# Optimization experiments

Hardware: AMD Instinct MI355X
Metric: run time of the kernel (lower is better)

Reference implementation:

```python
import jax, jax.numpy as jnp
import numpy as np
from jax import lax

B, H_IN, W_IN = 64, 480, 80
HID = 256                      # feature_dimension / 2
T = H_IN // 12                 # hidden_shape[0] = 40
I_GRU = (W_IN // 4) * 32       # hidden_shape[1] = 640


def setup_inputs() -> dict:
    key = jax.random.key(0)
    ks = jax.random.split(key, 20)
    rn = lambda k, s, sc: jax.random.normal(k, s, jnp.float32) * sc
    gs = 1.0 / np.sqrt(HID)    # torch GRU default init scale
    return {
        "input_image": jax.random.normal(ks[0], (B, 1, H_IN, W_IN), jnp.float32),
        "hidden": jnp.zeros((2, B, HID), jnp.float32),
        # conv weights: module uses randn*0.2 via init_conv_weights
        "conv0_w": rn(ks[1], (8, 1, 3, 3), 0.2),   "conv0_b": rn(ks[2], (8,), 0.05),
        "conv1_w": rn(ks[3], (16, 8, 3, 3), 0.2),  "conv1_b": rn(ks[4], (16,), 0.05),
        "conv2_w": rn(ks[5], (16, 16, 3, 3), 0.2), "conv2_b": rn(ks[6], (16,), 0.05),
        "conv3_w": rn(ks[7], (32, 16, 3, 3), 0.2), "conv3_b": rn(ks[8], (32,), 0.05),
        # GRU (1 layer, bidirectional). gate order: r, z, n (torch convention)
        "w_ih_f": rn(ks[9], (3 * HID, I_GRU), gs), "w_hh_f": rn(ks[10], (3 * HID, HID), gs),
        "b_ih_f": rn(ks[11], (3 * HID,), gs),      "b_hh_f": rn(ks[12], (3 * HID,), gs),
        "w_ih_b": rn(ks[13], (3 * HID, I_GRU), gs), "w_hh_b": rn(ks[14], (3 * HID, HID), gs),
        "b_ih_b": rn(ks[15], (3 * HID,), gs),       "b_hh_b": rn(ks[16], (3 * HID,), gs),
    }


def _conv(x, w, b):
    y = lax.conv_general_dilated(x, w, (1, 1), ((1, 1), (1, 1)),
                                 dimension_numbers=("NCHW", "OIHW", "NCHW"))
    return y + b[None, :, None, None]


def _maxpool(x, kh, kw):
    return lax.reduce_window(x, -jnp.inf, lax.max,
                             (1, 1, kh, kw), (1, 1, kh, kw), "VALID")


def _gru_dir(x_tbi, h0, w_ih, w_hh, b_ih, b_hh):
    # x_tbi: [T, B, I]; precompute input-side gates for all steps
    gx = jnp.einsum("tbi,gi->tbg", x_tbi, w_ih) + b_ih  # [T, B, 3H]

    def step(h, gx_t):
        gh = h @ w_hh.T + b_hh                            # [B, 3H]
        xr, xz, xn = jnp.split(gx_t, 3, axis=-1)
        hr, hz, hn = jnp.split(gh, 3, axis=-1)
        r = jax.nn.sigmoid(xr + hr)
        z = jax.nn.sigmoid(xz + hz)
        n = jnp.tanh(xn + r * hn)
        h_new = (1.0 - z) * n + z * h
        return h_new, h_new

    hT, ys = lax.scan(step, h0, gx)
    return ys, hT  # ys: [T, B, H]


def reference(input_image, hidden,
              conv0_w, conv0_b, conv1_w, conv1_b,
              conv2_w, conv2_b, conv3_w, conv3_b,
              w_ih_f, w_hh_f, b_ih_f, b_hh_f,
              w_ih_b, w_hh_b, b_ih_b, b_hh_b):
    y0 = jax.nn.relu(_conv(input_image, conv0_w, conv0_b))
    y1 = jax.nn.relu(_conv(y0, conv1_w, conv1_b))
    y2 = _maxpool(y1, 3, 2)
    y3 = jax.nn.relu(_conv(y2, conv2_w, conv2_b))
    y4 = jax.nn.relu(_conv(y3, conv3_w, conv3_b))
    y5 = _maxpool(y4, 4, 2)                     # [B, 32, T, W']
    b = y5.shape[0]
    # Python-loop reshape y_out[:, :, i] = y5[:, i%32, :, i//32]
    # is exactly a NCHW->NHWC permute followed by flattening (W', C):
    gru_in = jnp.transpose(y5, (0, 2, 3, 1)).reshape(b, T, I_GRU)
    x = jnp.transpose(gru_in, (1, 0, 2))        # [T, B, I]
    ys_f, hT_f = _gru_dir(x, hidden[0], w_ih_f, w_hh_f, b_ih_f, b_hh_f)
    ys_b, hT_b = _gru_dir(x[::-1], hidden[1], w_ih_b, w_hh_b, b_ih_b, b_hh_b)
    ys_b = ys_b[::-1]
    output = jnp.transpose(jnp.concatenate([ys_f, ys_b], axis=-1), (1, 0, 2))  # [B, T, 2H]
    hidden_out = jnp.stack([hT_f, hT_b], axis=0)                               # [2, B, H]
    return output, hidden_out
```

## Files before the change

kernel.cpp:

```cpp
#include <hip/hip_runtime.h>
#include <math.h>

static constexpr int B_   = 64;
static constexpr int H0_  = 480, W0_ = 80;
static constexpr int C0_  = 8, C1_ = 16, C2_ = 16, C3_ = 32;
static constexpr int H1_  = 160, W1_ = 40;
static constexpr int T_   = 40,  WP_ = 20;
static constexpr int IG_  = 640;
static constexpr int HID_ = 256;
static constexpr int G3_  = 768;
static constexpr int OUT_MAIN_ = B_ * T_ * 2 * HID_;
static constexpr int WSZ_ = G3_ * IG_;

typedef __attribute__((ext_vector_type(8))) short bf16x8;
typedef __attribute__((ext_vector_type(4))) short s16x4;
typedef __attribute__((ext_vector_type(4))) float f32x4;

__device__ inline short f2bf(float f) {
  unsigned u = __builtin_bit_cast(unsigned, f);
  u = (u + 0x7FFFu + ((u >> 16) & 1u)) >> 16;
  return (short)u;
}
__device__ inline float bf2f(short s) {
  return __builtin_bit_cast(float, ((unsigned)(unsigned short)s) << 16);
}
__device__ inline float sigm_(float x) { return 1.f / (1.f + __expf(-x)); }
__device__ inline float tanh_(float x) { return 1.f - 2.f / (1.f + __expf(2.f * x)); }

__device__ inline void split8(const float* p, bf16x8* hi, bf16x8* lo) {
  float4 u = *(const float4*)p, v = *(const float4*)(p + 4);
  float f[8] = {u.x, u.y, u.z, u.w, v.x, v.y, v.z, v.w};
  bf16x8 h, l;
#pragma unroll
  for (int i = 0; i < 8; ++i) {
    short hs = f2bf(f[i]);
    h[i] = hs;
    l[i] = f2bf(f[i] - bf2f(hs));
  }
  *hi = h; *lo = l;
}

__global__ __launch_bounds__(512, 4) void conv01_mfma(
    const float* __restrict__ img, const float* __restrict__ w0,
    const float* __restrict__ b0, const float* __restrict__ w1,
    const float* __restrict__ b1, float* __restrict__ y2) {
  __shared__ __align__(16) float im[16 * 84];
  __shared__ __align__(16) short y0h[14 * 82 * 8];
  __shared__ __align__(16) short y0l[14 * 82 * 8];
  int b = blockIdx.x / 40, tb = blockIdx.x % 40;
  int tid = threadIdx.x;
  int wave = tid >> 6, lane = tid & 63, q = lane >> 4, m15 = lane & 15;
  const float* imgb = img + (size_t)b * (H0_ * W0_);

  for (int i = tid; i < 16 * 84; i += 512) {
    int r = i / 84, col = i % 84;
    int gr = tb * 12 - 2 + r, gc = col - 2;
    float v = 0.f;
    if (gr >= 0 && gr < H0_ && gc >= 0 && gc < W0_) v = imgb[gr * W0_ + gc];
    im[i] = v;
  }
  bf16x8 w1hf[3], w1lf[3];
#pragma unroll
  for (int kt = 0; kt < 3; ++kt) {
    int p = kt * 4 + q;
    bf16x8 h, l;
#pragma unroll
    for (int e = 0; e < 8; ++e) {
      float w = (p < 9) ? w1[m15 * 72 + e * 9 + p] : 0.f;
      short hs = f2bf(w);
      h[e] = hs;
      l[e] = f2bf(w - bf2f(hs));
    }
    w1hf[kt] = h; w1lf[kt] = l;
  }
  float b1c = b1[m15];
  __syncthreads();

  {
    int ci = tid & 7;
    float wv0[9];
#pragma unroll
    for (int k = 0; k < 9; ++k) wv0[k] = w0[ci * 9 + k];
    float b0c = b0[ci];
#pragma unroll 1
    for (int i = tid; i < 14 * 82 * 8; i += 512) {
      int rest = i >> 3;
      int lc = rest % 82, r = rest / 82;
      int grow = tb * 12 - 1 + r, gc = lc - 1;
      float v = 0.f;
      if (grow >= 0 && grow < H0_ && gc >= 0 && gc < W0_) {
        float s = b0c;
#pragma unroll
        for (int kh = 0; kh < 3; ++kh)
#pragma unroll
          for (int kw = 0; kw < 3; ++kw)
            s += im[(r + kh) * 84 + lc + kw] * wv0[kh * 3 + kw];
        v = fmaxf(s, 0.f);
      }
      short hs = f2bf(v);
      y0h[i] = hs;
      y0l[i] = f2bf(v - bf2f(hs));
    }
  }
  __syncthreads();

#pragma unroll 1
  for (int j = wave; j < 20; j += 8) {
    int pr = j / 5, ct = j % 5;
    f32x4 pmax = {0.f, 0.f, 0.f, 0.f};
#pragma unroll
    for (int rr2 = 0; rr2 < 3; ++rr2) {
      int o = pr * 3 + rr2;
      f32x4 acc = {0.f, 0.f, 0.f, 0.f};
#pragma unroll
      for (int kt = 0; kt < 3; ++kt) {
        int p = kt * 4 + q;
        int pp = (p < 9) ? p : 8;
        int kh = pp / 3, kw = pp % 3;
        int ar = ((o + kh) * 82 + ct * 16 + m15 + kw) * 8;
        bf16x8 ah = *(const bf16x8*)&y0h[ar];
        bf16x8 al = *(const bf16x8*)&y0l[ar];
        acc = __builtin_amdgcn_mfma_f32_16x16x32_bf16(al, w1hf[kt], acc, 0, 0, 0);
        acc = __builtin_amdgcn_mfma_f32_16x16x32_bf16(ah, w1lf[kt], acc, 0, 0, 0);
        acc = __builtin_amdgcn_mfma_f32_16x16x32_bf16(ah, w1hf[kt], acc, 0, 0, 0);
      }
#pragma unroll
      for (int r = 0; r < 4; ++r)
        pmax[r] = fmaxf(pmax[r], fmaxf(acc[r] + b1c, 0.f));
    }
    int R = tb * 4 + pr;
    size_t base = (((size_t)b * 160 + R) * 40 + ct * 8 + q * 2) * 16 + m15;
    y2[base] = fmaxf(pmax[0], pmax[1]);
    y2[base + 16] = fmaxf(pmax[2], pmax[3]);
  }
}

__global__ __launch_bounds__(512, 2) void conv23_mfma(
    const float* __restrict__ y2, const float* __restrict__ w2,
    const float* __restrict__ b2, const float* __restrict__ w3,
    const float* __restrict__ b3, short* __restrict__ xh,
    short* __restrict__ xl) {
  __shared__ __align__(16) short y2h[20 * 42 * 16], y2l[20 * 42 * 16];
  __shared__ __align__(16) short y3h[18 * 42 * 16], y3l[18 * 42 * 16];
  int b = blockIdx.x / 10, tb = blockIdx.x % 10;
  int tid = threadIdx.x;
  int wave = tid >> 6, lane = tid & 63, q = lane >> 4, m15 = lane & 15;
  int ci0 = (q & 1) * 8;

  for (int i = tid; i < 20 * 42 * 4; i += 512) {
    int ci4 = i & 3;
    int rest = i >> 2;
    int lc = rest % 42, r = rest / 42;
    int gr = tb * 16 - 2 + r, gc = lc - 1;
    float4 v = {0.f, 0.f, 0.f, 0.f};
    if (gr >= 0 && gr < 160 && gc >= 0 && gc < 40)
      v = *(const float4*)&y2[(((size_t)b * 160 + gr) * 40 + gc) * 16 + ci4 * 4];
    float f[4] = {v.x, v.y, v.z, v.w};
    s16x4 hv, lv;
#pragma unroll
    for (int e = 0; e < 4; ++e) {
      short hs = f2bf(f[e]);
      hv[e] = hs;
      lv[e] = f2bf(f[e] - bf2f(hs));
    }
    int idx = (r * 42 + lc) * 16 + ci4 * 4;
    *(s16x4*)&y2h[idx] = hv;
    *(s16x4*)&y2l[idx] = lv;
  }
  for (int i = tid; i < 18 * 2 * 16; i += 512) {
    int rr = i / 32, sl = i % 32;
    int col = (sl >> 4) * 41, ch = sl & 15;
    y3h[(rr * 42 + col) * 16 + ch] = 0;
    y3l[(rr * 42 + col) * 16 + ch] = 0;
  }
  bf16x8 w2hf[5], w2lf[5];
#pragma unroll
  for (int kt = 0; kt < 5; ++kt) {
    int p = 2 * kt + (q >> 1);
    bf16x8 h, l;
#pragma unroll
    for (int e = 0; e < 8; ++e) {
      float w = (p < 9) ? w2[(m15 * 16 + ci0 + e) * 9 + p] : 0.f;
      short hs = f2bf(w);
      h[e] = hs;
      l[e] = f2bf(w - bf2f(hs));
    }
    w2hf[kt] = h; w2lf[kt] = l;
  }
  float b2c = b2[m15];
  __syncthreads();

#pragma unroll 1
  for (int i = wave; i < 54; i += 8) {
    int rr = i / 3, ct = i % 3;
    f32x4 acc = {0.f, 0.f, 0.f, 0.f};
#pragma unroll
    for (int kt = 0; kt < 5; ++kt) {
      int p = 2 * kt + (q >> 1);
      int pp = (p < 9) ? p : 8;
      int kh = pp / 3, kw = pp % 3;
      int lc = min(ct * 16 + m15 + kw, 41);
      int ar = ((rr + kh) * 42 + lc) * 16 + ci0;
      bf16x8 ah = *(const bf16x8*)&y2h[ar];
      bf16x8 al = *(const bf16x8*)&y2l[ar];
      acc = __builtin_amdgcn_mfma_f32_16x16x32_bf16(al, w2hf[kt], acc, 0, 0, 0);
      acc = __builtin_amdgcn_mfma_f32_16x16x32_bf16(ah, w2lf[kt], acc, 0, 0, 0);
      acc = __builtin_amdgcn_mfma_f32_16x16x32_bf16(ah, w2hf[kt], acc, 0, 0, 0);
    }
    int grow = tb * 16 - 1 + rr;
    bool rowok = (grow >= 0 && grow < 160);
#pragma unroll
    for (int r = 0; r < 4; ++r) {
      int col = ct * 16 + q * 4 + r;
      if (col < 40) {
        float v = rowok ? fmaxf(acc[r] + b2c, 0.f) : 0.f;
        short hs = f2bf(v);
        int di = (rr * 42 + 1 + col) * 16 + m15;
        y3h[di] = hs;
        y3l[di] = f2bf(v - bf2f(hs));
      }
    }
  }
  __syncthreads();

  int nt = wave & 1, pl = wave >> 1;
  bf16x8 w3hf[5], w3lf[5];
#pragma unroll
  for (int kt = 0; kt < 5; ++kt) {
    int p = 2 * kt + (q >> 1);
    bf16x8 h, l;
#pragma unroll
    for (int e = 0; e < 8; ++e) {
      float w = (p < 9) ? w3[((nt * 16 + m15) * 16 + ci0 + e) * 9 + p] : 0.f;
      short hs = f2bf(w);
      h[e] = hs;
      l[e] = f2bf(w - bf2f(hs));
    }
    w3hf[kt] = h; w3lf[kt] = l;
  }
  float b3c = b3[nt * 16 + m15];

#pragma unroll 1
  for (int ct = 0; ct < 3; ++ct) {
    f32x4 pmax = {0.f, 0.f, 0.f, 0.f};
#pragma unroll
    for (int rr2 = 0; rr2 < 4; ++rr2) {
      int o = pl * 4 + rr2;
      f32x4 acc = {0.f, 0.f, 0.f, 0.f};
#pragma unroll
      for (int kt = 0; kt < 5; ++kt) {
        int p = 2 * kt + (q >> 1);
        int pp = (p < 9) ? p : 8;
        int kh = pp / 3, kw = pp % 3;
        int lc = min(ct * 16 + m15 + kw, 41);
        int ar = ((o + kh) * 42 + lc) * 16 + ci0;
        bf16x8 ah = *(const bf16x8*)&y3h[ar];
        bf16x8 al = *(const bf16x8*)&y3l[ar];
        acc = __builtin_amdgcn_mfma_f32_16x16x32_bf16(al, w3hf[kt], acc, 0, 0, 0);
        acc = __builtin_amdgcn_mfma_f32_16x16x32_bf16(ah, w3lf[kt], acc, 0, 0, 0);
        acc = __builtin_amdgcn_mfma_f32_16x16x32_bf16(ah, w3hf[kt], acc, 0, 0, 0);
      }
#pragma unroll
      for (int r = 0; r < 4; ++r) {
        float v = fmaxf(acc[r] + b3c, 0.f);
        pmax[r] = fmaxf(pmax[r], v);
      }
    }
    if (ct < 2 || q < 2) {
      int t = tb * 4 + pl;
      int wo = ct * 8 + q * 2;
      size_t base = (((size_t)t * 64 + b) * 20 + wo) * 32 + nt * 16 + m15;
      float v0 = fmaxf(pmax[0], pmax[1]);
      float v1 = fmaxf(pmax[2], pmax[3]);
      short s0 = f2bf(v0), s1 = f2bf(v1);
      xh[base] = s0;       xl[base] = f2bf(v0 - bf2f(s0));
      xh[base + 32] = s1;  xl[base + 32] = f2bf(v1 - bf2f(s1));
    }
  }
}

__global__ __launch_bounds__(256) void split_w(
    const float* __restrict__ wf, const float* __restrict__ wb,
    short* __restrict__ Wh, short* __restrict__ Wl) {
  int i = blockIdx.x * 256 + threadIdx.x;
  const float* src = (i < 61440) ? (wf + (size_t)i * 8)
                                 : (wb + (size_t)(i - 61440) * 8);
  bf16x8 h, l;
  split8(src, &h, &l);
  *(bf16x8*)&Wh[(size_t)i * 8] = h;
  *(bf16x8*)&Wl[(size_t)i * 8] = l;
}

__global__ __launch_bounds__(256) void gemm_gx_mfma(
    const short* __restrict__ xh, const short* __restrict__ xl,
    const short* __restrict__ Wh, const short* __restrict__ Wl,
    const float* __restrict__ bih_f, const float* __restrict__ bih_b,
    const float* __restrict__ bhh_f, const float* __restrict__ bhh_b,
    float* __restrict__ gx) {
  __shared__ __align__(16) short Ah[4 * 128 * 8], Al[4 * 128 * 8];
  __shared__ __align__(16) short Bh[4 * 128 * 8], Bl[4 * 128 * 8];
  int bm = blockIdx.x * 128, bn = blockIdx.y * 128, dir = blockIdx.z;
  const short* Whd = Wh + (size_t)dir * WSZ_;
  const short* Wld = Wl + (size_t)dir * WSZ_;
  const float* bias = dir ? bih_b : bih_f;
  const float* bias2 = dir ? bhh_b : bhh_f;
  float* C = gx + (size_t)dir * (T_ * B_) * G3_;
  int tid = threadIdx.x;
  int wave = tid >> 6, lane = tid & 63, q = lane >> 4, n = lane & 15;
  int wm = (wave & 1) * 64, wn2 = (wave >> 1) * 64;
  f32x4 acc[4][4];
#pragma unroll
  for (int mi = 0; mi < 4; ++mi)
#pragma unroll
    for (int ni = 0; ni < 4; ++ni) acc[mi][ni] = (f32x4){0.f, 0.f, 0.f, 0.f};

  for (int k0 = 0; k0 < IG_; k0 += 32) {
    int ks = k0 + wave * 8;
    *(bf16x8*)&Ah[(wave * 128 + lane) * 8] =
        *(const bf16x8*)&xh[(size_t)(bm + lane) * IG_ + ks];
    *(bf16x8*)&Al[(wave * 128 + lane) * 8] =
        *(const bf16x8*)&xl[(size_t)(bm + lane) * IG_ + ks];
    *(bf16x8*)&Ah[(wave * 128 + lane + 64) * 8] =
        *(const bf16x8*)&xh[(size_t)(bm + lane + 64) * IG_ + ks];
    *(bf16x8*)&Al[(wave * 128 + lane + 64) * 8] =
        *(const bf16x8*)&xl[(size_t)(bm + lane + 64) * IG_ + ks];
    *(bf16x8*)&Bh[(wave * 128 + lane) * 8] =
        *(const bf16x8*)&Whd[(size_t)(bn + lane) * IG_ + ks];
    *(bf16x8*)&Bl[(wave * 128 + lane) * 8] =
        *(const bf16x8*)&Wld[(size_t)(bn + lane) * IG_ + ks];
    *(bf16x8*)&Bh[(wave * 128 + lane + 64) * 8] =
        *(const bf16x8*)&Whd[(size_t)(bn + lane + 64) * IG_ + ks];
    *(bf16x8*)&Bl[(wave * 128 + lane + 64) * 8] =
        *(const bf16x8*)&Wld[(size_t)(bn + lane + 64) * IG_ + ks];
    __syncthreads();
    bf16x8 ah[4], al[4], bh[4], bl[4];
#pragma unroll
    for (int mi = 0; mi < 4; ++mi) {
      ah[mi] = *(const bf16x8*)&Ah[(q * 128 + wm + mi * 16 + n) * 8];
      al[mi] = *(const bf16x8*)&Al[(q * 128 + wm + mi * 16 + n) * 8];
    }
#pragma unroll
    for (int ni = 0; ni < 4; ++ni) {
      bh[ni] = *(const bf16x8*)&Bh[(q * 128 + wn2 + ni * 16 + n) * 8];
      bl[ni] = *(const bf16x8*)&Bl[(q * 128 + wn2 + ni * 16 + n) * 8];
    }
#pragma unroll
    for (int mi = 0; mi < 4; ++mi)
#pragma unroll
      for (int ni = 0; ni < 4; ++ni) {
        acc[mi][ni] = __builtin_amdgcn_mfma_f32_16x16x32_bf16(
            al[mi], bh[ni], acc[mi][ni], 0, 0, 0);
        acc[mi][ni] = __builtin_amdgcn_mfma_f32_16x16x32_bf16(
            ah[mi], bl[ni], acc[mi][ni], 0, 0, 0);
        acc[mi][ni] = __builtin_amdgcn_mfma_f32_16x16x32_bf16(
            ah[mi], bh[ni], acc[mi][ni], 0, 0, 0);
      }
    __syncthreads();
  }
#pragma unroll
  for (int mi = 0; mi < 4; ++mi)
#pragma unroll
    for (int ni = 0; ni < 4; ++ni)
#pragma unroll
      for (int r = 0; r < 4; ++r) {
        int row = bm + wm + mi * 16 + q * 4 + r;
        int col = bn + wn2 + ni * 16 + n;
        float bb = bias[col] + (col < 512 ? bias2[col] : 0.f);
        C[(size_t)row * G3_ + col] = acc[mi][ni][r] + bb;
      }
}

__global__ __launch_bounds__(1024) void gru_mfma(
    const float* __restrict__ gx,
    const float* __restrict__ whh_f, const float* __restrict__ whh_b,
    const float* __restrict__ bhh_f, const float* __restrict__ bhh_b,
    const float* __restrict__ h0, float* __restrict__ out) {
  __shared__ __align__(16) short wn[32 * 256 * 8];
  __shared__ __align__(16) short hb[2][32 * 16 * 8];
  int blk = blockIdx.x, dir = blk >> 2, mb = blk & 3;
  const float* Wh  = dir ? whh_b : whh_f;
  const float* bhh = dir ? bhh_b : bhh_f;
  int tid = threadIdx.x;
  int wave = tid >> 6, lane = tid & 63, q = lane >> 4, n = lane & 15;
  int jw = wave << 4;

  for (int idx = tid; idx < 256 * 32; idx += 1024) {
    int j = idx >> 5, ch = idx & 31;
    const float* src = Wh + (size_t)(512 + j) * HID_ + ch * 8;
    float4 u = *(const float4*)src, v = *(const float4*)(src + 4);
    short* d = &wn[(ch * 256 + j) * 8];
    d[0] = f2bf(u.x); d[1] = f2bf(u.y); d[2] = f2bf(u.z); d[3] = f2bf(u.w);
    d[4] = f2bf(v.x); d[5] = f2bf(v.y); d[6] = f2bf(v.z); d[7] = f2bf(v.w);
  }
  if (tid < 512) {
    int b = tid >> 5, ch = tid & 31;
    const float* src = h0 + (size_t)(dir * 64 + mb * 16 + b) * HID_ + ch * 8;
    float4 u = *(const float4*)src, v = *(const float4*)(src + 4);
    short* d = &hb[0][(ch * 16 + b) * 8];
    d[0] = f2bf(u.x); d[1] = f2bf(u.y); d[2] = f2bf(u.z); d[3] = f2bf(u.w);
    d[4] = f2bf(v.x); d[5] = f2bf(v.y); d[6] = f2bf(v.z); d[7] = f2bf(v.w);
  }
  bf16x8 Br[8], Bz[8];
#pragma unroll
  for (int kt = 0; kt < 8; ++kt) {
    const float* pr = Wh + (size_t)(jw + n) * HID_ + kt * 32 + q * 8;
    const float* pz = Wh + (size_t)(256 + jw + n) * HID_ + kt * 32 + q * 8;
    float4 u = *(const float4*)pr, v = *(const float4*)(pr + 4);
    Br[kt] = (bf16x8){f2bf(u.x), f2bf(u.y), f2bf(u.z), f2bf(u.w),
                      f2bf(v.x), f2bf(v.y), f2bf(v.z), f2bf(v.w)};
    float4 uz = *(const float4*)pz, vz = *(const float4*)(pz + 4);
    Bz[kt] = (bf16x8){f2bf(uz.x), f2bf(uz.y), f2bf(uz.z), f2bf(uz.w),
                      f2bf(vz.x), f2bf(vz.y), f2bf(vz.z), f2bf(vz.w)};
  }
  float hold[4];
#pragma unroll
  for (int r = 0; r < 4; ++r)
    hold[r] = h0[(size_t)(dir * 64 + mb * 16 + q * 4 + r) * HID_ + jw + n];
  float bh2 = bhh[512 + jw + n];
  int chc = (jw + n) >> 3, ce = (jw + n) & 7;

  float xr[4], xz[4], xn[4];
  {
    int t0 = dir ? (T_ - 1) : 0;
    const float* gxt = gx + ((size_t)(dir * T_ + t0) * B_ + mb * 16) * G3_;
#pragma unroll
    for (int r = 0; r < 4; ++r) {
      const float* gxb = gxt + (size_t)(q * 4 + r) * G3_ + jw + n;
      xr[r] = gxb[0]; xz[r] = gxb[256]; xn[r] = gxb[512];
    }
  }
  __syncthreads();

  for (int s = 0; s < T_; ++s) {
    int t = dir ? (T_ - 1 - s) : s;
    const short* hc = hb[s & 1];
    short* hx = hb[(s & 1) ^ 1];

    float pxr[4], pxz[4], pxn[4];
    {
      int sn = (s + 1 < T_) ? s + 1 : s;
      int tn = dir ? (T_ - 1 - sn) : sn;
      const float* gxt = gx + ((size_t)(dir * T_ + tn) * B_ + mb * 16) * G3_;
#pragma unroll
      for (int r = 0; r < 4; ++r) {
        const float* gxb = gxt + (size_t)(q * 4 + r) * G3_ + jw + n;
        pxr[r] = gxb[0]; pxz[r] = gxb[256]; pxn[r] = gxb[512];
      }
    }

    f32x4 a0 = {0.f, 0.f, 0.f, 0.f}, a1 = a0, a2 = a0;
#pragma unroll
    for (int kt = 0; kt < 8; ++kt) {
      bf16x8 af = *(const bf16x8*)&hc[((kt * 4 + q) * 16 + n) * 8];
      bf16x8 bn = *(const bf16x8*)&wn[((kt * 4 + q) * 256 + jw + n) * 8];
      a0 = __builtin_amdgcn_mfma_f32_16x16x32_bf16(af, Br[kt], a0, 0, 0, 0);
      a1 = __builtin_amdgcn_mfma_f32_16x16x32_bf16(af, Bz[kt], a1, 0, 0, 0);
      a2 = __builtin_amdgcn_mfma_f32_16x16x32_bf16(af, bn, a2, 0, 0, 0);
    }
#pragma unroll
    for (int r = 0; r < 4; ++r) {
      float rg = sigm_(xr[r] + a0[r]);
      float zg = sigm_(xz[r] + a1[r]);
      float ng = tanh_(xn[r] + rg * (a2[r] + bh2));
      float hnew = (1.f - zg) * ng + zg * hold[r];
      hold[r] = hnew;
      int gb = mb * 16 + q * 4 + r;
      out[((size_t)gb * T_ + t) * (2 * HID_) + dir * HID_ + jw + n] = hnew;
      hx[(chc * 16 + q * 4 + r) * 8 + ce] = f2bf(hnew);
    }
#pragma unroll
    for (int r = 0; r < 4; ++r) {
      xr[r] = pxr[r]; xz[r] = pxz[r]; xn[r] = pxn[r];
    }
    asm volatile("s_waitcnt lgkmcnt(0)\n\ts_barrier" ::: "memory");
  }
#pragma unroll
  for (int r = 0; r < 4; ++r)
    out[(size_t)OUT_MAIN_ + (size_t)(dir * 64 + mb * 16 + q * 4 + r) * HID_ + jw + n] = hold[r];
}

extern "C" void kernel_launch(void* const* d_in, const int* in_sizes, int n_in,
                              void* d_out, int out_size, void* d_ws, size_t ws_size,
                              hipStream_t stream) {
  (void)in_sizes; (void)n_in; (void)out_size; (void)ws_size;
  const float* img    = (const float*)d_in[0];
  const float* hid0   = (const float*)d_in[1];
  const float* c0w    = (const float*)d_in[2];
  const float* c0b    = (const float*)d_in[3];
  const float* c1w    = (const float*)d_in[4];
  const float* c1b    = (const float*)d_in[5];
  const float* c2w    = (const float*)d_in[6];
  const float* c2b    = (const float*)d_in[7];
  const float* c3w    = (const float*)d_in[8];
  const float* c3b    = (const float*)d_in[9];
  const float* wih_f  = (const float*)d_in[10];
  const float* whh_f  = (const float*)d_in[11];
  const float* bih_f  = (const float*)d_in[12];
  const float* bhh_f  = (const float*)d_in[13];
  const float* wih_b  = (const float*)d_in[14];
  const float* whh_b  = (const float*)d_in[15];
  const float* bih_b  = (const float*)d_in[16];
  const float* bhh_b  = (const float*)d_in[17];
  float* out = (float*)d_out;

  float* wsf = (float*)d_ws;
  float* y2  = wsf;
  short* xh  = (short*)(wsf + 6553600);
  short* xl  = xh + 1638400;
  float* gx  = wsf + 8192000;
  short* Wh  = (short*)wsf;
  short* Wl  = Wh + 983040;

  conv01_mfma<<<64 * 40, 512, 0, stream>>>(img, c0w, c0b, c1w, c1b, y2);
  conv23_mfma<<<64 * 10, 512, 0, stream>>>(y2, c2w, c2b, c3w, c3b, xh, xl);
  split_w<<<480, 256, 0, stream>>>(wih_f, wih_b, Wh, Wl);
  gemm_gx_mfma<<<dim3(20, 6, 2), 256, 0, stream>>>(xh, xl, Wh, Wl, bih_f, bih_b,
                                                   bhh_f, bhh_b, gx);
  gru_mfma<<<8, 1024, 0, stream>>>(gx, whh_f, whh_b, bhh_f, bhh_b, hid0, out);
}
```

Baseline: 407.5 us.

## Double-buffer gx GEMM LDS tiles and vectorize conv0 register blocking

The input-projection GEMM now uses two LDS buffers. It prefetches the next K-slice into registers while the MFMAs run on the current slice, which removes one barrier per iteration and hides global load latency. Separately, conv0 in the fused conv kernel now computes four adjacent output columns per thread from float4 loads of a padded 88-wide image tile, cutting LDS reads. The cost is doubled LDS for the GEMM and more registers, which may lower occupancy.

```diff
diff --git a/kernel.cpp b/kernel.cpp
--- a/kernel.cpp
+++ b/kernel.cpp
@@ -44,7 +44,7 @@
     const float* __restrict__ img, const float* __restrict__ w0,
     const float* __restrict__ b0, const float* __restrict__ w1,
     const float* __restrict__ b1, float* __restrict__ y2) {
-  __shared__ __align__(16) float im[16 * 84];
+  __shared__ __align__(16) float im[16 * 88];
   __shared__ __align__(16) short y0h[14 * 82 * 8];
   __shared__ __align__(16) short y0l[14 * 82 * 8];
   int b = blockIdx.x / 40, tb = blockIdx.x % 40;
@@ -52,8 +52,8 @@
   int wave = tid >> 6, lane = tid & 63, q = lane >> 4, m15 = lane & 15;
   const float* imgb = img + (size_t)b * (H0_ * W0_);
 
-  for (int i = tid; i < 16 * 84; i += 512) {
-    int r = i / 84, col = i % 84;
+  for (int i = tid; i < 16 * 88; i += 512) {
+    int r = i / 88, col = i % 88;
     int gr = tb * 12 - 2 + r, gc = col - 2;
     float v = 0.f;
     if (gr >= 0 && gr < H0_ && gc >= 0 && gc < W0_) v = imgb[gr * W0_ + gc];
@@ -83,23 +83,40 @@
     for (int k = 0; k < 9; ++k) wv0[k] = w0[ci * 9 + k];
     float b0c = b0[ci];
 #pragma unroll 1
-    for (int i = tid; i < 14 * 82 * 8; i += 512) {
+    for (int i = tid; i < 14 * 21 * 8; i += 512) {
       int rest = i >> 3;
-      int lc = rest % 82, r = rest / 82;
-      int grow = tb * 12 - 1 + r, gc = lc - 1;
-      float v = 0.f;
-      if (grow >= 0 && grow < H0_ && gc >= 0 && gc < W0_) {
-        float s = b0c;
-#pragma unroll
-        for (int kh = 0; kh < 3; ++kh)
-#pragma unroll
-          for (int kw = 0; kw < 3; ++kw)
-            s += im[(r + kh) * 84 + lc + kw] * wv0[kh * 3 + kw];
-        v = fmaxf(s, 0.f);
-      }
-      short hs = f2bf(v);
-      y0h[i] = hs;
-      y0l[i] = f2bf(v - bf2f(hs));
+      int g = rest % 21, r = rest / 21;
+      int grow = tb * 12 - 1 + r;
+      bool rowok = (grow >= 0 && grow < H0_);
+      float ra[3][8];
+#pragma unroll
+      for (int kh = 0; kh < 3; ++kh) {
+        float4 u = *(const float4*)&im[(r + kh) * 88 + 4 * g];
+        float4 v = *(const float4*)&im[(r + kh) * 88 + 4 * g + 4];
+        ra[kh][0] = u.x; ra[kh][1] = u.y; ra[kh][2] = u.z; ra[kh][3] = u.w;
+        ra[kh][4] = v.x; ra[kh][5] = v.y; ra[kh][6] = v.z; ra[kh][7] = v.w;
+      }
+#pragma unroll
+      for (int c = 0; c < 4; ++c) {
+        int lc = 4 * g + c;
+        if (lc < 82) {
+          int gc = lc - 1;
+          float vv = 0.f;
+          if (rowok && gc >= 0 && gc < W0_) {
+            float s = b0c;
+#pragma unroll
+            for (int kh = 0; kh < 3; ++kh)
+#pragma unroll
+              for (int kw = 0; kw < 3; ++kw)
+                s += ra[kh][c + kw] * wv0[kh * 3 + kw];
+            vv = fmaxf(s, 0.f);
+          }
+          short hs = f2bf(vv);
+          int di = (r * 82 + lc) * 8 + ci;
+          y0h[di] = hs;
+          y0l[di] = f2bf(vv - bf2f(hs));
+        }
+      }
     }
   }
   __syncthreads();
@@ -297,8 +314,8 @@
     const float* __restrict__ bih_f, const float* __restrict__ bih_b,
     const float* __restrict__ bhh_f, const float* __restrict__ bhh_b,
     float* __restrict__ gx) {
-  __shared__ __align__(16) short Ah[4 * 128 * 8], Al[4 * 128 * 8];
-  __shared__ __align__(16) short Bh[4 * 128 * 8], Bl[4 * 128 * 8];
+  __shared__ __align__(16) short Ah[2][4 * 128 * 8], Al[2][4 * 128 * 8];
+  __shared__ __align__(16) short Bh[2][4 * 128 * 8], Bl[2][4 * 128 * 8];
   int bm = blockIdx.x * 128, bn = blockIdx.y * 128, dir = blockIdx.z;
   const short* Whd = Wh + (size_t)dir * WSZ_;
   const short* Wld = Wl + (size_t)dir * WSZ_;
@@ -314,35 +331,48 @@
 #pragma unroll
     for (int ni = 0; ni < 4; ++ni) acc[mi][ni] = (f32x4){0.f, 0.f, 0.f, 0.f};
 
-  for (int k0 = 0; k0 < IG_; k0 += 32) {
-    int ks = k0 + wave * 8;
-    *(bf16x8*)&Ah[(wave * 128 + lane) * 8] =
-        *(const bf16x8*)&xh[(size_t)(bm + lane) * IG_ + ks];
-    *(bf16x8*)&Al[(wave * 128 + lane) * 8] =
-        *(const bf16x8*)&xl[(size_t)(bm + lane) * IG_ + ks];
-    *(bf16x8*)&Ah[(wave * 128 + lane + 64) * 8] =
-        *(const bf16x8*)&xh[(size_t)(bm + lane + 64) * IG_ + ks];
-    *(bf16x8*)&Al[(wave * 128 + lane + 64) * 8] =
-        *(const bf16x8*)&xl[(size_t)(bm + lane + 64) * IG_ + ks];
-    *(bf16x8*)&Bh[(wave * 128 + lane) * 8] =
-        *(const bf16x8*)&Whd[(size_t)(bn + lane) * IG_ + ks];
-    *(bf16x8*)&Bl[(wave * 128 + lane) * 8] =
-        *(const bf16x8*)&Wld[(size_t)(bn + lane) * IG_ + ks];
-    *(bf16x8*)&Bh[(wave * 128 + lane + 64) * 8] =
-        *(const bf16x8*)&Whd[(size_t)(bn + lane + 64) * IG_ + ks];
-    *(bf16x8*)&Bl[(wave * 128 + lane + 64) * 8] =
-        *(const bf16x8*)&Wld[(size_t)(bn + lane + 64) * IG_ + ks];
-    __syncthreads();
+  const short* xh0 = &xh[(size_t)(bm + lane) * IG_ + wave * 8];
+  const short* xl0 = &xl[(size_t)(bm + lane) * IG_ + wave * 8];
+  const short* xh1 = &xh[(size_t)(bm + lane + 64) * IG_ + wave * 8];
+  const short* xl1 = &xl[(size_t)(bm + lane + 64) * IG_ + wave * 8];
+  const short* wh0 = &Whd[(size_t)(bn + lane) * IG_ + wave * 8];
+  const short* wl0 = &Wld[(size_t)(bn + lane) * IG_ + wave * 8];
+  const short* wh1 = &Whd[(size_t)(bn + lane + 64) * IG_ + wave * 8];
+  const short* wl1 = &Wld[(size_t)(bn + lane + 64) * IG_ + wave * 8];
+  int s0 = (wave * 128 + lane) * 8, s1 = (wave * 128 + lane + 64) * 8;
+
+  {
+    *(bf16x8*)&Ah[0][s0] = *(const bf16x8*)xh0;
+    *(bf16x8*)&Al[0][s0] = *(const bf16x8*)xl0;
+    *(bf16x8*)&Ah[0][s1] = *(const bf16x8*)xh1;
+    *(bf16x8*)&Al[0][s1] = *(const bf16x8*)xl1;
+    *(bf16x8*)&Bh[0][s0] = *(const bf16x8*)wh0;
+    *(bf16x8*)&Bl[0][s0] = *(const bf16x8*)wl0;
+    *(bf16x8*)&Bh[0][s1] = *(const bf16x8*)wh1;
+    *(bf16x8*)&Bl[0][s1] = *(const bf16x8*)wl1;
+  }
+  __syncthreads();
+
+  for (int t = 0; t < 20; ++t) {
+    int cur = t & 1;
+    bf16x8 ra0, rl0, ra1, rl1, rb0, rm0, rb1, rm1;
+    if (t < 19) {
+      int ko = (t + 1) * 32;
+      ra0 = *(const bf16x8*)(xh0 + ko); rl0 = *(const bf16x8*)(xl0 + ko);
+      ra1 = *(const bf16x8*)(xh1 + ko); rl1 = *(const bf16x8*)(xl1 + ko);
+      rb0 = *(const bf16x8*)(wh0 + ko); rm0 = *(const bf16x8*)(wl0 + ko);
+      rb1 = *(const bf16x8*)(wh1 + ko); rm1 = *(const bf16x8*)(wl1 + ko);
+    }
     bf16x8 ah[4], al[4], bh[4], bl[4];
 #pragma unroll
     for (int mi = 0; mi < 4; ++mi) {
-      ah[mi] = *(const bf16x8*)&Ah[(q * 128 + wm + mi * 16 + n) * 8];
-      al[mi] = *(const bf16x8*)&Al[(q * 128 + wm + mi * 16 + n) * 8];
+      ah[mi] = *(const bf16x8*)&Ah[cur][(q * 128 + wm + mi * 16 + n) * 8];
+      al[mi] = *(const bf16x8*)&Al[cur][(q * 128 + wm + mi * 16 + n) * 8];
     }
 #pragma unroll
     for (int ni = 0; ni < 4; ++ni) {
-      bh[ni] = *(const bf16x8*)&Bh[(q * 128 + wn2 + ni * 16 + n) * 8];
-      bl[ni] = *(const bf16x8*)&Bl[(q * 128 + wn2 + ni * 16 + n) * 8];
+      bh[ni] = *(const bf16x8*)&Bh[cur][(q * 128 + wn2 + ni * 16 + n) * 8];
+      bl[ni] = *(const bf16x8*)&Bl[cur][(q * 128 + wn2 + ni * 16 + n) * 8];
     }
 #pragma unroll
     for (int mi = 0; mi < 4; ++mi)
@@ -355,6 +385,13 @@
         acc[mi][ni] = __builtin_amdgcn_mfma_f32_16x16x32_bf16(
             ah[mi], bh[ni], acc[mi][ni], 0, 0, 0);
       }
+    if (t < 19) {
+      int nb = cur ^ 1;
+      *(bf16x8*)&Ah[nb][s0] = ra0; *(bf16x8*)&Al[nb][s0] = rl0;
+      *(bf16x8*)&Ah[nb][s1] = ra1; *(bf16x8*)&Al[nb][s1] = rl1;
+      *(bf16x8*)&Bh[nb][s0] = rb0; *(bf16x8*)&Bl[nb][s0] = rm0;
+      *(bf16x8*)&Bh[nb][s1] = rb1; *(bf16x8*)&Bl[nb][s1] = rm1;
+    }
     __syncthreads();
   }
 #pragma unroll
```

Result: no change. 408.6 us (+0.3%).
